# Kernel tuning notes

Hardware: AMD Instinct MI355X
Metric: run time of the kernel (lower is better)

Reference implementation:

```python
import jax, jax.numpy as jnp
import numpy as np

EPS = 1e-5

def _conv1x1(x, w):
    # x: (B, Cin, N, K), w: (Cout, Cin) -> (B, Cout, N, K)
    return jnp.einsum('oc,bcnk->bonk', w, x)

def _bn2d(x, gamma, beta):
    # eval-mode BN with running_mean=0, running_var=1 (fresh init)
    scale = gamma / jnp.sqrt(1.0 + EPS)
    return x * scale[None, :, None, None] + beta[None, :, None, None]

def setup_inputs() -> dict:
    key = jax.random.key(0)
    ks = jax.random.split(key, 10)
    B, Cin, N, K = 8, 64, 1024, 32
    Cout, M = 64, 8
    Cin2 = 2 * Cin  # kernel_input='w_neighbor'
    features = jax.random.normal(ks[0], (B, Cin, N, K), dtype=jnp.float32)
    points_xyz = jax.random.normal(ks[1], (B, 3, N, K), dtype=jnp.float32)
    # ScoreNet convs: mlp_channels [7,16,16,16,M]; first 3 have BN (no bias), last has bias
    w1 = jax.random.normal(ks[2], (16, 7), dtype=jnp.float32) * (2.0 / 7) ** 0.5
    w2 = jax.random.normal(ks[3], (16, 16), dtype=jnp.float32) * (2.0 / 16) ** 0.5
    w3 = jax.random.normal(ks[4], (16, 16), dtype=jnp.float32) * (2.0 / 16) ** 0.5
    w4 = jax.random.normal(ks[5], (M, 16), dtype=jnp.float32) * (2.0 / 16) ** 0.5
    b4 = jnp.zeros((M,), dtype=jnp.float32)
    g1 = jnp.ones((16,), jnp.float32); be1 = jnp.zeros((16,), jnp.float32)
    g2 = jnp.ones((16,), jnp.float32); be2 = jnp.zeros((16,), jnp.float32)
    g3 = jnp.ones((16,), jnp.float32); be3 = jnp.zeros((16,), jnp.float32)
    # weight bank: kaiming_normal on (M, 2Cin, Cout) -> stored as (2Cin, M, Cout)
    wb = jax.random.normal(ks[6], (Cin2, M, Cout), dtype=jnp.float32) * (2.0 / Cin2) ** 0.5
    bn_g = jnp.ones((Cout,), jnp.float32); bn_b = jnp.zeros((Cout,), jnp.float32)
    return dict(features=features, points_xyz=points_xyz,
                w1=w1, g1=g1, be1=be1, w2=w2, g2=g2, be2=be2,
                w3=w3, g3=g3, be3=be3, w4=w4, b4=b4,
                weight_bank=wb, bn_g=bn_g, bn_b=bn_b)

def reference(features, points_xyz, w1, g1, be1, w2, g2, be2, w3, g3, be3,
              w4, b4, weight_bank, bn_g, bn_b):
    B, Cin, N, K = features.shape
    M = weight_bank.shape[1]
    # kernel_input = 'w_neighbor': concat(feat - center, feat) -> (B, 2Cin, N, K)
    center_f = features[..., :1]
    feat = jnp.concatenate([features - center_f, features], axis=1)
    # scorenet input = 'w_neighbor_dist': (center_xyz, xyz_diff, dist) -> (B, 7, N, K)
    center_xyz = jnp.broadcast_to(points_xyz[..., :1], points_xyz.shape)
    xyz_diff = points_xyz - center_xyz
    dist = jnp.sqrt(jnp.sum(xyz_diff * xyz_diff, axis=1, keepdims=True))
    xyz_feats = jnp.concatenate([center_xyz, xyz_diff, dist], axis=1)
    h = jax.nn.relu(_bn2d(_conv1x1(xyz_feats, w1), g1, be1))
    h = jax.nn.relu(_bn2d(_conv1x1(h, w2), g2, be2))
    h = jax.nn.relu(_bn2d(_conv1x1(h, w3), g3, be3))
    s = _conv1x1(h, w4) + b4[None, :, None, None]  # (B, M, N, K)
    scores = jax.nn.softmax(s, axis=1)
    scores = jnp.transpose(scores, (0, 2, 3, 1))  # (B, N, K, M)
    # matmul with weight bank then score-weighted sum over kernels, fused via einsum
    # original: (B,N,K,2Cin)@(2Cin,M*Cout) -> (B,N,K,M,Cout); sum_m scores * . -> (B,N,K,Cout)
    new_features = jnp.einsum('bcnk,cmo,bnkm->bonk', feat, weight_bank, scores)
    # BN2d (eval, fresh stats) + ReLU
    new_features = jax.nn.relu(_bn2d(new_features, bn_g, bn_b))
    return new_features
```

## Files before the change

kernel.cpp:

```cpp
#include <hip/hip_runtime.h>
#include <hip/hip_bf16.h>

typedef _Float16 f16;
typedef __attribute__((ext_vector_type(2))) _Float16 f16x2;
typedef __attribute__((ext_vector_type(8))) _Float16 f16x8;
typedef __attribute__((ext_vector_type(16))) float f32x16;

#define BNSCL 0.9999950000375f

__global__ __launch_bounds__(256) void k_scores(
    const float* __restrict__ xyz,
    const float* __restrict__ w1, const float* __restrict__ g1, const float* __restrict__ be1,
    const float* __restrict__ w2, const float* __restrict__ g2, const float* __restrict__ be2,
    const float* __restrict__ w3, const float* __restrict__ g3, const float* __restrict__ be3,
    const float* __restrict__ w4, const float* __restrict__ b4,
    const float* __restrict__ wb, f16* __restrict__ wbtA,
    f16* __restrict__ scores)
{
    __shared__ float lw[856];
    const int tid = threadIdx.x;

    if (blockIdx.x < 256) {
        int idx = blockIdx.x * 256 + tid;
        int j    = idx & 7;
        int lane = (idx >> 3) & 63;
        int ks   = (idx >> 9) & 63;
        int ot   = idx >> 15;
        int cp   = ks * 2 + (lane >> 5);
        int o    = ot * 32 + (lane & 31);
        wbtA[idx] = (f16)wb[(cp * 8 + j) * 64 + o];
    }

    if (tid < 112) lw[tid] = w1[tid];
    lw[112 + tid] = w2[tid];
    lw[368 + tid] = w3[tid];
    if (tid < 128) lw[624 + tid] = w4[tid];
    if (tid < 8)   lw[752 + tid] = b4[tid];
    if (tid < 16) {
        lw[760 + tid] = g1[tid] * BNSCL;  lw[776 + tid] = be1[tid];
        lw[792 + tid] = g2[tid] * BNSCL;  lw[808 + tid] = be2[tid];
        lw[824 + tid] = g3[tid] * BNSCL;  lw[840 + tid] = be3[tid];
    }
    __syncthreads();

    float in7[2][7], h1[2][16], h2[2][16], s[2][8];

#pragma unroll
    for (int q = 0; q < 2; ++q) {
        int g = blockIdx.x * 512 + q * 256 + tid;
        int b = g >> 15;
        int p = g & 32767;
        int pc = p & ~31;
        const float* xb = xyz + (size_t)b * 98304;
        float cx = xb[pc], cy = xb[32768 + pc], cz = xb[65536 + pc];
        float dx = xb[p] - cx, dy = xb[32768 + p] - cy, dz = xb[65536 + p] - cz;
        in7[q][0] = cx; in7[q][1] = cy; in7[q][2] = cz;
        in7[q][3] = dx; in7[q][4] = dy; in7[q][5] = dz;
        in7[q][6] = sqrtf(dx * dx + dy * dy + dz * dz);
    }

#pragma unroll
    for (int o = 0; o < 16; ++o) {
        float a0 = 0.f, a1 = 0.f;
#pragma unroll
        for (int c = 0; c < 7; ++c) {
            float w = lw[o * 7 + c];
            a0 += w * in7[0][c]; a1 += w * in7[1][c];
        }
        float gs = lw[760 + o], bb = lw[776 + o];
        h1[0][o] = fmaxf(a0 * gs + bb, 0.f);
        h1[1][o] = fmaxf(a1 * gs + bb, 0.f);
    }
#pragma unroll
    for (int o = 0; o < 16; ++o) {
        float a0 = 0.f, a1 = 0.f;
#pragma unroll
        for (int c = 0; c < 16; ++c) {
            float w = lw[112 + o * 16 + c];
            a0 += w * h1[0][c]; a1 += w * h1[1][c];
        }
        float gs = lw[792 + o], bb = lw[808 + o];
        h2[0][o] = fmaxf(a0 * gs + bb, 0.f);
        h2[1][o] = fmaxf(a1 * gs + bb, 0.f);
    }
#pragma unroll
    for (int o = 0; o < 16; ++o) {
        float a0 = 0.f, a1 = 0.f;
#pragma unroll
        for (int c = 0; c < 16; ++c) {
            float w = lw[368 + o * 16 + c];
            a0 += w * h2[0][c]; a1 += w * h2[1][c];
        }
        float gs = lw[824 + o], bb = lw[840 + o];
        h1[0][o] = fmaxf(a0 * gs + bb, 0.f);
        h1[1][o] = fmaxf(a1 * gs + bb, 0.f);
    }
#pragma unroll
    for (int o = 0; o < 8; ++o) {
        float bb = lw[752 + o];
        float a0 = bb, a1 = bb;
#pragma unroll
        for (int c = 0; c < 16; ++c) {
            float w = lw[624 + o * 16 + c];
            a0 += w * h1[0][c]; a1 += w * h1[1][c];
        }
        s[0][o] = a0; s[1][o] = a1;
    }

#pragma unroll
    for (int q = 0; q < 2; ++q) {
        int g = blockIdx.x * 512 + q * 256 + tid;
        float mx = s[q][0];
#pragma unroll
        for (int i = 1; i < 8; ++i) mx = fmaxf(mx, s[q][i]);
        float sum = 0.f;
#pragma unroll
        for (int i = 0; i < 8; ++i) { s[q][i] = __expf(s[q][i] - mx); sum += s[q][i]; }
        float inv = 1.f / sum;
        f16x8 o8;
#pragma unroll
        for (int i = 0; i < 8; ++i) o8[i] = (f16)(s[q][i] * inv);
        *(f16x8*)(scores + (size_t)g * 8) = o8;
    }
}

__global__ __launch_bounds__(1024, 4) void k_main(
    const float* __restrict__ feat,
    const f16* __restrict__ scores,
    const f16* __restrict__ wbtA,
    const float* __restrict__ bn_g, const float* __restrict__ bn_b,
    float* __restrict__ out)
{
    __shared__ __align__(16) f16 lwb[32768];
    __shared__ __align__(16) float fbuf[8][2][1024];

    const int tid  = threadIdx.x;
    const int lane = tid & 63;
    const int wave = tid >> 6;
    const int l31  = lane & 31;
    const int lh   = lane >> 5;
    const int w64  = wave * 64;

    const int ot = blockIdx.x >> 8;
    const int g  = blockIdx.x & 255;
    const int pblock = g * 1024;
    const int b    = pblock >> 15;
    const int pt0  = (pblock & 32767) + w64;
    const int pc0  = pt0 + l31;
    const int pc1  = pc0 + 32;

    const float* fb = feat + (size_t)b * 2097152;
    const float* gsrc0 = fb + (pblock & 32767) + w64 + lane;

    const f16* src = wbtA + ((size_t)ot << 15);
#pragma unroll
    for (int it = 0; it < 4; ++it) {
        int idx = it * 1024 + tid;
        *(int4*)&lwb[idx << 3] = *(const int4*)&src[idx << 3];
    }

    const int gpt = pblock + w64 + l31;
    f16x8 sv0 = *(const f16x8*)(scores + (size_t)gpt * 8);
    f16x8 sv1 = *(const f16x8*)(scores + (size_t)(gpt + 32) * 8);
    const f16x2 s0a = {sv0[0], sv0[1]}, s0b = {sv0[2], sv0[3]},
                s0c = {sv0[4], sv0[5]}, s0d = {sv0[6], sv0[7]};
    const f16x2 s1a = {sv1[0], sv1[1]}, s1b = {sv1[2], sv1[3]},
                s1c = {sv1[4], sv1[5]}, s1d = {sv1[6], sv1[7]};

    f32x16 acc0 = {}, acc1 = {};
    const f16* Alds = lwb + (lane << 3);

#define STAGE(t)                                                               \
    {                                                                          \
        __builtin_amdgcn_global_load_lds(                                      \
            (const __attribute__((address_space(1))) void*)                    \
                (gsrc0 + ((size_t)(2 * (t)) << 15)),                           \
            (__attribute__((address_space(3))) void*)&fbuf[(t) & 7][0][w64],   \
            4, 0, 0);                                                          \
        __builtin_amdgcn_global_load_lds(                                      \
            (const __attribute__((address_space(1))) void*)                    \
                (gsrc0 + ((size_t)(2 * (t) + 1) << 15)),                       \
            (__attribute__((address_space(3))) void*)&fbuf[(t) & 7][1][w64],   \
            4, 0, 0);                                                          \
    }

#define WAITV(n) asm volatile("s_waitcnt vmcnt(" #n ")" ::: "memory")

    __builtin_amdgcn_sched_barrier(0);
    STAGE(0); STAGE(1); STAGE(2); STAGE(3); STAGE(4); STAGE(5);

    asm volatile("s_waitcnt lgkmcnt(0)" ::: "memory");
    __builtin_amdgcn_s_barrier();

#define KSTEP(kk)                                                              \
    {                                                                          \
        f16x8 aD = *(const f16x8*)(Alds + ((size_t)(kk) << 9));                \
        f16x8 aR = *(const f16x8*)(Alds + ((size_t)((kk) + 32) << 9));         \
        const float* frow = fbuf[(kk) & 7][lh];                                \
        float fv0 = frow[w64 + l31], fv1 = frow[w64 + l31 + 32];               \
        float fc0 = frow[w64],       fc1 = frow[w64 + 32];                     \
        f16 hR0 = (f16)fv0,          hR1 = (f16)fv1;                           \
        f16 hD0 = (f16)(fv0 - fc0),  hD1 = (f16)(fv1 - fc1);                   \
        f16x2 fR0 = {hR0, hR0}, fR1 = {hR1, hR1};                              \
        f16x2 fD0 = {hD0, hD0}, fD1 = {hD1, hD1};                              \
        f16x2 d0a = fD0 * s0a, d0b = fD0 * s0b, d0c = fD0 * s0c, d0d = fD0 * s0d; \
        f16x2 d1a = fD1 * s1a, d1b = fD1 * s1b, d1c = fD1 * s1c, d1d = fD1 * s1d; \
        f16x2 r0a = fR0 * s0a, r0b = fR0 * s0b, r0c = fR0 * s0c, r0d = fR0 * s0d; \
        f16x2 r1a = fR1 * s1a, r1b = fR1 * s1b, r1c = fR1 * s1c, r1d = fR1 * s1d; \
        f16x8 bD0 = {d0a[0],d0a[1],d0b[0],d0b[1],d0c[0],d0c[1],d0d[0],d0d[1]}; \
        f16x8 bD1 = {d1a[0],d1a[1],d1b[0],d1b[1],d1c[0],d1c[1],d1d[0],d1d[1]}; \
        f16x8 bR0 = {r0a[0],r0a[1],r0b[0],r0b[1],r0c[0],r0c[1],r0d[0],r0d[1]}; \
        f16x8 bR1 = {r1a[0],r1a[1],r1b[0],r1b[1],r1c[0],r1c[1],r1d[0],r1d[1]}; \
        acc0 = __builtin_amdgcn_mfma_f32_32x32x16_f16(aD, bD0, acc0, 0, 0, 0); \
        acc1 = __builtin_amdgcn_mfma_f32_32x32x16_f16(aD, bD1, acc1, 0, 0, 0); \
        acc0 = __builtin_amdgcn_mfma_f32_32x32x16_f16(aR, bR0, acc0, 0, 0, 0); \
        acc1 = __builtin_amdgcn_mfma_f32_32x32x16_f16(aR, bR1, acc1, 0, 0, 0); \
    }

#define PAIR(p)                                                                \
    STAGE(2 * (p) + 6) STAGE(2 * (p) + 7)                                      \
    WAITV(12);                                                                 \
    KSTEP(2 * (p)) KSTEP(2 * (p) + 1)

    PAIR(0)  PAIR(1)  PAIR(2)  PAIR(3)
    PAIR(4)  PAIR(5)  PAIR(6)  PAIR(7)
    PAIR(8)  PAIR(9)  PAIR(10) PAIR(11)
    PAIR(12)
    WAITV(8);
    KSTEP(26) KSTEP(27)
    WAITV(4);
    KSTEP(28) KSTEP(29)
    WAITV(0);
    KSTEP(30) KSTEP(31)
#undef PAIR
#undef KSTEP
#undef STAGE
#undef WAITV

    __builtin_amdgcn_sched_barrier(0);

#pragma unroll
    for (int r = 0; r < 16; ++r) {
        int o = ot * 32 + (r & 3) + ((r >> 2) << 3) + (lh << 2);
        float gs = bn_g[o] * BNSCL, bb = bn_b[o];
        size_t row = (size_t)(b * 64 + o) << 15;
        out[row + pc0] = fmaxf(acc0[r] * gs + bb, 0.f);
        out[row + pc1] = fmaxf(acc1[r] * gs + bb, 0.f);
    }
}

extern "C" void kernel_launch(void* const* d_in, const int* in_sizes, int n_in,
                              void* d_out, int out_size, void* d_ws, size_t ws_size,
                              hipStream_t stream)
{
    const float* features = (const float*)d_in[0];
    const float* xyz      = (const float*)d_in[1];
    const float* w1  = (const float*)d_in[2];
    const float* g1  = (const float*)d_in[3];
    const float* be1 = (const float*)d_in[4];
    const float* w2  = (const float*)d_in[5];
    const float* g2  = (const float*)d_in[6];
    const float* be2 = (const float*)d_in[7];
    const float* w3  = (const float*)d_in[8];
    const float* g3  = (const float*)d_in[9];
    const float* be3 = (const float*)d_in[10];
    const float* w4  = (const float*)d_in[11];
    const float* b4  = (const float*)d_in[12];
    const float* wb  = (const float*)d_in[13];
    const float* bn_g = (const float*)d_in[14];
    const float* bn_b = (const float*)d_in[15];

    f16* scores = (f16*)d_ws;
    f16* wbtA   = (f16*)((char*)d_ws + (4u << 20));

    k_scores<<<512, 256, 0, stream>>>(xyz, w1, g1, be1, w2, g2, be2,
                                      w3, g3, be3, w4, b4, wb, wbtA, scores);
    k_main<<<512, 1024, 0, stream>>>(features, scores, wbtA, bn_g, bn_b,
                                     (float*)d_out);
}
```

Baseline: 178.9 us.

## Fold diff-branch weights into combined bank and apply center correction via small MFMA

The concat(feat-center, feat) input is rewritten algebraically: the weight bank's two halves are pre-summed so each k-step needs only two score-weighted MFMAs on raw features instead of four. The center-feature contribution is accumulated separately in a third accumulator using masked one-hot B operands, then spilled to shared scratch and applied as a final correction MFMA against the scores. This removes per-step subtraction and half of the packed multiplies, at the cost of extra scratch LDS, an epilogue pass, and summing two weights in fp16 before multiplication.

```diff
diff --git a/kernel.cpp b/kernel.cpp
--- a/kernel.cpp
+++ b/kernel.cpp
@@ -24,11 +24,14 @@
         int idx = blockIdx.x * 256 + tid;
         int j    = idx & 7;
         int lane = (idx >> 3) & 63;
-        int ks   = (idx >> 9) & 63;
+        int ks   = (idx >> 9) & 31;
+        int bank = (idx >> 14) & 1;
         int ot   = idx >> 15;
-        int cp   = ks * 2 + (lane >> 5);
+        int c    = ks * 2 + (lane >> 5);
         int o    = ot * 32 + (lane & 31);
-        wbtA[idx] = (f16)wb[(cp * 8 + j) * 64 + o];
+        float vD = wb[(c * 8 + j) * 64 + o];
+        float v  = bank ? vD : vD + wb[((c + 64) * 8 + j) * 64 + o];
+        wbtA[idx] = (f16)v;
     }
 
     if (tid < 112) lw[tid] = w1[tid];
@@ -133,6 +136,7 @@
 {
     __shared__ __align__(16) f16 lwb[32768];
     __shared__ __align__(16) float fbuf[8][2][1024];
+    __shared__ __align__(16) f16 gscr[16][512];
 
     const int tid  = threadIdx.x;
     const int lane = tid & 63;
@@ -167,7 +171,18 @@
     const f16x2 s1a = {sv1[0], sv1[1]}, s1b = {sv1[2], sv1[3]},
                 s1c = {sv1[4], sv1[5]}, s1d = {sv1[6], sv1[7]};
 
-    f32x16 acc0 = {}, acc1 = {};
+    const bool mon  = (l31 < 16);
+    const int  mpos = l31 & 7;
+    const f16x2 mk0 = { (f16)((mon && mpos == 0) ? 1.f : 0.f),
+                        (f16)((mon && mpos == 1) ? 1.f : 0.f) };
+    const f16x2 mk1 = { (f16)((mon && mpos == 2) ? 1.f : 0.f),
+                        (f16)((mon && mpos == 3) ? 1.f : 0.f) };
+    const f16x2 mk2 = { (f16)((mon && mpos == 4) ? 1.f : 0.f),
+                        (f16)((mon && mpos == 5) ? 1.f : 0.f) };
+    const f16x2 mk3 = { (f16)((mon && mpos == 6) ? 1.f : 0.f),
+                        (f16)((mon && mpos == 7) ? 1.f : 0.f) };
+
+    f32x16 acc0 = {}, acc1 = {}, accG = {};
     const f16* Alds = lwb + (lane << 3);
 
 #define STAGE(t)                                                               \
@@ -194,27 +209,23 @@
 
 #define KSTEP(kk)                                                              \
     {                                                                          \
-        f16x8 aD = *(const f16x8*)(Alds + ((size_t)(kk) << 9));                \
-        f16x8 aR = *(const f16x8*)(Alds + ((size_t)((kk) + 32) << 9));         \
+        f16x8 aS = *(const f16x8*)(Alds + ((size_t)(kk) << 9));                \
+        f16x8 aD = *(const f16x8*)(Alds + ((size_t)((kk) + 32) << 9));         \
         const float* frow = fbuf[(kk) & 7][lh];                                \
         float fv0 = frow[w64 + l31], fv1 = frow[w64 + l31 + 32];               \
         float fc0 = frow[w64],       fc1 = frow[w64 + 32];                     \
-        f16 hR0 = (f16)fv0,          hR1 = (f16)fv1;                           \
-        f16 hD0 = (f16)(fv0 - fc0),  hD1 = (f16)(fv1 - fc1);                   \
-        f16x2 fR0 = {hR0, hR0}, fR1 = {hR1, hR1};                              \
-        f16x2 fD0 = {hD0, hD0}, fD1 = {hD1, hD1};                              \
-        f16x2 d0a = fD0 * s0a, d0b = fD0 * s0b, d0c = fD0 * s0c, d0d = fD0 * s0d; \
-        f16x2 d1a = fD1 * s1a, d1b = fD1 * s1b, d1c = fD1 * s1c, d1d = fD1 * s1d; \
+        float fcs = (l31 & 8) ? fc1 : fc0;                                     \
+        f16 hR0 = (f16)fv0, hR1 = (f16)fv1, hC = (f16)(-fcs);                  \
+        f16x2 fR0 = {hR0, hR0}, fR1 = {hR1, hR1}, fg2 = {hC, hC};              \
         f16x2 r0a = fR0 * s0a, r0b = fR0 * s0b, r0c = fR0 * s0c, r0d = fR0 * s0d; \
         f16x2 r1a = fR1 * s1a, r1b = fR1 * s1b, r1c = fR1 * s1c, r1d = fR1 * s1d; \
-        f16x8 bD0 = {d0a[0],d0a[1],d0b[0],d0b[1],d0c[0],d0c[1],d0d[0],d0d[1]}; \
-        f16x8 bD1 = {d1a[0],d1a[1],d1b[0],d1b[1],d1c[0],d1c[1],d1d[0],d1d[1]}; \
-        f16x8 bR0 = {r0a[0],r0a[1],r0b[0],r0b[1],r0c[0],r0c[1],r0d[0],r0d[1]}; \
-        f16x8 bR1 = {r1a[0],r1a[1],r1b[0],r1b[1],r1c[0],r1c[1],r1d[0],r1d[1]}; \
-        acc0 = __builtin_amdgcn_mfma_f32_32x32x16_f16(aD, bD0, acc0, 0, 0, 0); \
-        acc1 = __builtin_amdgcn_mfma_f32_32x32x16_f16(aD, bD1, acc1, 0, 0, 0); \
-        acc0 = __builtin_amdgcn_mfma_f32_32x32x16_f16(aR, bR0, acc0, 0, 0, 0); \
-        acc1 = __builtin_amdgcn_mfma_f32_32x32x16_f16(aR, bR1, acc1, 0, 0, 0); \
+        f16x2 q0 = mk0 * fg2, q1 = mk1 * fg2, q2 = mk2 * fg2, q3 = mk3 * fg2;  \
+        f16x8 bS0 = {r0a[0],r0a[1],r0b[0],r0b[1],r0c[0],r0c[1],r0d[0],r0d[1]}; \
+        f16x8 bS1 = {r1a[0],r1a[1],r1b[0],r1b[1],r1c[0],r1c[1],r1d[0],r1d[1]}; \
+        f16x8 bG  = {q0[0],q0[1],q1[0],q1[1],q2[0],q2[1],q3[0],q3[1]};         \
+        acc0 = __builtin_amdgcn_mfma_f32_32x32x16_f16(aS, bS0, acc0, 0, 0, 0); \
+        acc1 = __builtin_amdgcn_mfma_f32_32x32x16_f16(aS, bS1, acc1, 0, 0, 0); \
+        accG = __builtin_amdgcn_mfma_f32_32x32x16_f16(aD, bG, accG, 0, 0, 0);  \
     }
 
 #define PAIR(p)                                                                \
@@ -236,6 +247,25 @@
 #undef KSTEP
 #undef STAGE
 #undef WAITV
+
+    if (l31 < 16) {
+        const int base = (l31 >> 3) * 256 + (l31 & 7);
+#pragma unroll
+        for (int r = 0; r < 16; ++r) {
+            int o = (r & 3) + ((r >> 2) << 3) + (lh << 2);
+            gscr[wave][base + o * 8] = (f16)accG[r];
+        }
+    }
+    asm volatile("s_waitcnt lgkmcnt(0)" ::: "memory");
+    __builtin_amdgcn_sched_barrier(0);
+    {
+        f16x8 a2 = *(const f16x8*)&gscr[wave][lh * 256 + l31 * 8];
+        f16x8 z8 = {};
+        f16x8 bC0 = lh ? z8 : sv0;
+        f16x8 bC1 = lh ? sv1 : z8;
+        acc0 = __builtin_amdgcn_mfma_f32_32x32x16_f16(a2, bC0, acc0, 0, 0, 0);
+        acc1 = __builtin_amdgcn_mfma_f32_32x32x16_f16(a2, bC1, acc1, 0, 0, 0);
+    }
 
     __builtin_amdgcn_sched_barrier(0);
 
```

After: 171.0 us. -4.4%, faster.
